# Kernel optimization log

Hardware: AMD Instinct MI355X
Metric: run time of the kernel (lower is better)

## Reference

```python
import jax, jax.numpy as jnp
import numpy as np

N_NODES = 100000
N_EDGES = 625000
D_FEAT = 128
OUT_DIM = 128


def setup_inputs() -> dict:
    key = jax.random.key(0)
    k1, k2, k3, k4 = jax.random.split(key, 4)
    feature = jax.random.normal(k1, (N_NODES, D_FEAT), dtype=jnp.float32)
    relation_weight = jax.random.uniform(k2, (N_EDGES, 1), dtype=jnp.float32)
    # row 0: destination (segment) ids, row 1: source (gather) ids
    relation_indices = jax.random.randint(k3, (2, N_EDGES), 0, N_NODES, dtype=jnp.int32)
    W = jax.random.normal(k4, (2 * D_FEAT, OUT_DIM), dtype=jnp.float32) * 0.05
    b = jnp.zeros((OUT_DIM,), dtype=jnp.float32)
    return {"feature": feature, "relation_weight": relation_weight, "W": W, "b": b,
            "relation_indices": relation_indices}


def reference(feature, relation_weight, W, b, relation_indices):
    dst = relation_indices[0]  # segment ids [E]
    src = relation_indices[1]  # gather ids  [E]
    n = feature.shape[0]
    # message: gather neighbor features and weight per edge  [E, D]
    feat_n = feature[src] * relation_weight
    # segment mean over destination nodes (dropout_rate=0.0 -> identity)
    seg_sum = jax.ops.segment_sum(feat_n, dst, num_segments=n)          # [N, D]
    seg_cnt = jax.ops.segment_sum(jnp.ones((src.shape[0], 1), feat_n.dtype), dst,
                                  num_segments=n)                        # [N, 1]
    neigh_mean = seg_sum / jnp.maximum(seg_cnt, 1.0)
    # concat self + aggregated, dense update (activation/normalization = None)
    h = jnp.concatenate([feature, neigh_mean], axis=-1)                  # [N, 2D]
    return h @ W + b
```

## Files before the change

### kernel.cpp

```cpp
#include <hip/hip_runtime.h>

constexpr int N   = 100000;
constexpr int E   = 625000;
constexpr int DF  = 128;
constexpr int CAP = 32;

typedef __attribute__((ext_vector_type(8))) _Float16 f16x8;
typedef __attribute__((ext_vector_type(2))) __fp16 fp16x2_raw;
typedef __attribute__((ext_vector_type(4))) float f32x4;

__device__ inline unsigned pkh(float lo, float hi) {
    union { fp16x2_raw h; unsigned u; } c;
    c.h = __builtin_amdgcn_cvt_pkrtz(lo, hi);
    return c.u;
}

__device__ inline int swz(int row, int byteInRow) {
    return row * 128 + (byteInRow ^ ((row & 7) << 4));
}

__global__ __launch_bounds__(256) void prep(
    const float* __restrict__ feature, const float* __restrict__ W,
    int* __restrict__ cnt, unsigned short* __restrict__ wtb,
    unsigned short* __restrict__ fh)
{
    int t = blockIdx.x * 256 + threadIdx.x;
    int stride = gridDim.x * 256;
    for (int i = t; i < N; i += stride) cnt[i] = 0;
    for (int i = t; i < 256 * 64; i += stride) {
        int k = (2 * i) >> 7, c = (2 * i) & 127;
        float a = W[2 * i], b = W[2 * i + 1];
        wtb[(c)     * 256 + k] = (unsigned short)(pkh(a, a) & 0xFFFF);
        wtb[(c + 1) * 256 + k] = (unsigned short)(pkh(b, b) & 0xFFFF);
    }
    int n8 = N * DF / 8;
    for (int i = t; i < n8; i += stride) {
        float4 a = reinterpret_cast<const float4*>(feature)[2 * i];
        float4 b = reinterpret_cast<const float4*>(feature)[2 * i + 1];
        uint4 o;
        o.x = pkh(a.x, a.y); o.y = pkh(a.z, a.w);
        o.z = pkh(b.x, b.y); o.w = pkh(b.z, b.w);
        reinterpret_cast<uint4*>(fh)[i] = o;
    }
}

__global__ __launch_bounds__(256) void direct_bucket(
    const int* __restrict__ dst, const int* __restrict__ src,
    const float* __restrict__ rw,
    int* __restrict__ cnt, int2* pad)
{
    int e = blockIdx.x * 256 + threadIdx.x;
    if (e < E) {
        int d = dst[e];
        int p = atomicAdd(&cnt[d], 1);
        if (p < CAP) pad[d * CAP + p] = make_int2(src[e], __float_as_int(rw[e]));
    }
}

__global__ __launch_bounds__(256) void aggregate(
    const unsigned short* __restrict__ fh,
    const int2* pad, const int* __restrict__ cnt,
    unsigned short* nbf)
{
    int node = blockIdx.x * 4 + (threadIdx.x >> 6);
    if (node >= N) return;
    int lane = threadIdx.x & 63;
    int eslot = lane >> 4;
    int chunk = lane & 15;
    int deg = cnt[node];
    int degc = min(deg, CAP);
    const int2* ep = pad + (size_t)node * CAP;
    const uint4* fh4 = reinterpret_cast<const uint4*>(fh);

    float acc[8];
    #pragma unroll
    for (int q = 0; q < 8; ++q) acc[q] = 0.f;

    int i = eslot;
    int2 sw0 = (i     < degc) ? ep[i]     : make_int2(0, 0);
    int2 sw1 = (i + 4 < degc) ? ep[i + 4] : make_int2(0, 0);
    while (i < degc) {
        union { uint4 u; _Float16 h[8]; } c0, c1;
        c0.u = fh4[(size_t)sw0.x * 16 + chunk];
        c1.u = fh4[(size_t)sw1.x * 16 + chunk];
        int2 sw0n = (i + 8  < degc) ? ep[i + 8]  : make_int2(0, 0);
        int2 sw1n = (i + 12 < degc) ? ep[i + 12] : make_int2(0, 0);
        float w0 = __int_as_float(sw0.y);
        float w1 = __int_as_float(sw1.y);
        #pragma unroll
        for (int q = 0; q < 8; ++q) acc[q] = fmaf((float)c0.h[q], w0, acc[q]);
        #pragma unroll
        for (int q = 0; q < 8; ++q) acc[q] = fmaf((float)c1.h[q], w1, acc[q]);
        i += 8; sw0 = sw0n; sw1 = sw1n;
    }
    #pragma unroll
    for (int q = 0; q < 8; ++q) {
        acc[q] += __shfl_xor(acc[q], 16, 64);
        acc[q] += __shfl_xor(acc[q], 32, 64);
    }
    if (lane < 16) {
        float inv = 1.0f / fmaxf((float)deg, 1.0f);
        uint4 o;
        o.x = pkh(acc[0] * inv, acc[1] * inv);
        o.y = pkh(acc[2] * inv, acc[3] * inv);
        o.z = pkh(acc[4] * inv, acc[5] * inv);
        o.w = pkh(acc[6] * inv, acc[7] * inv);
        reinterpret_cast<uint4*>(nbf)[(size_t)node * 16 + chunk] = o;
    }
}

__global__ __launch_bounds__(256) void sage_gemm(
    const unsigned short* __restrict__ fh, const unsigned short* __restrict__ nbf,
    const unsigned short* __restrict__ wtb,
    const float* __restrict__ bias, float* __restrict__ out)
{
    __shared__ short As[128 * 64];
    __shared__ short Bs[128 * 64];

    const int tid = threadIdx.x;
    const int lane = tid & 63;
    const int wv = tid >> 6;
    const int wr = (wv >> 1) * 64;
    const int wc = (wv & 1) * 64;
    const int l15 = lane & 15;
    const int lg  = lane >> 4;
    const int rowBase = blockIdx.x * 128;

    f32x4 acc[4][4];
    #pragma unroll
    for (int mi = 0; mi < 4; ++mi)
        #pragma unroll
        for (int ni = 0; ni < 4; ++ni)
            acc[mi][ni] = f32x4{0.f, 0.f, 0.f, 0.f};

    #pragma unroll
    for (int kc = 0; kc < 4; ++kc) {
        const int kglob = kc * 64;
        const unsigned short* Aap = (kc < 2) ? fh : nbf;
        const int kbase = (kc & 1) * 64;
        #pragma unroll
        for (int it = 0; it < 4; ++it) {
            int i = it * 256 + tid;
            int r  = i >> 3;
            int c8 = i & 7;
            int grow = rowBase + r;
            int4 v = {0, 0, 0, 0};
            if (grow < N)
                v = *reinterpret_cast<const int4*>(&Aap[(size_t)grow * DF + kbase + c8 * 8]);
            *reinterpret_cast<int4*>(reinterpret_cast<char*>(As) + swz(r, c8 * 16)) = v;
        }
        #pragma unroll
        for (int it = 0; it < 4; ++it) {
            int i = it * 256 + tid;
            int c  = i >> 3;
            int k8 = i & 7;
            int4 v = *reinterpret_cast<const int4*>(&wtb[(size_t)c * 256 + kglob + k8 * 8]);
            *reinterpret_cast<int4*>(reinterpret_cast<char*>(Bs) + swz(c, k8 * 16)) = v;
        }
        __syncthreads();

        #pragma unroll
        for (int kk = 0; kk < 2; ++kk) {
            const int kb = kk * 64;
            f16x8 af[4], bfr[4];
            #pragma unroll
            for (int mi = 0; mi < 4; ++mi) {
                int row = wr + mi * 16 + l15;
                af[mi] = *reinterpret_cast<const f16x8*>(
                    reinterpret_cast<const char*>(As) + swz(row, kb + lg * 16));
            }
            #pragma unroll
            for (int ni = 0; ni < 4; ++ni) {
                int col = wc + ni * 16 + l15;
                bfr[ni] = *reinterpret_cast<const f16x8*>(
                    reinterpret_cast<const char*>(Bs) + swz(col, kb + lg * 16));
            }
            #pragma unroll
            for (int mi = 0; mi < 4; ++mi)
                #pragma unroll
                for (int ni = 0; ni < 4; ++ni)
                    acc[mi][ni] = __builtin_amdgcn_mfma_f32_16x16x32_f16(
                        af[mi], bfr[ni], acc[mi][ni], 0, 0, 0);
        }
        __syncthreads();
    }

    #pragma unroll
    for (int ni = 0; ni < 4; ++ni) {
        int col = wc + ni * 16 + l15;
        float bc = bias[col];
        #pragma unroll
        for (int mi = 0; mi < 4; ++mi) {
            #pragma unroll
            for (int q = 0; q < 4; ++q) {
                int grow = rowBase + wr + mi * 16 + lg * 4 + q;
                if (grow < N) out[(size_t)grow * 128 + col] = acc[mi][ni][q] + bc;
            }
        }
    }
}

extern "C" void kernel_launch(void* const* d_in, const int* in_sizes, int n_in,
                              void* d_out, int out_size, void* d_ws, size_t ws_size,
                              hipStream_t stream) {
    const float* feature = (const float*)d_in[0];
    const float* rw      = (const float*)d_in[1];
    const float* W       = (const float*)d_in[2];
    const float* bias    = (const float*)d_in[3];
    const int*   ridx    = (const int*)d_in[4];
    const int*   dst     = ridx;
    const int*   src     = ridx + E;
    float* out = (float*)d_out;

    unsigned short* fh  = (unsigned short*)d_ws;
    int2*           pad = (int2*)(fh + (size_t)N * DF);
    unsigned short* nbf = (unsigned short*)pad;
    int*            cnt = (int*)((char*)pad + (size_t)N * CAP * 8);
    unsigned short* wtb = (unsigned short*)(cnt + N);

    prep<<<1280, 256, 0, stream>>>(feature, W, cnt, wtb, fh);
    direct_bucket<<<(E + 255) / 256, 256, 0, stream>>>(dst, src, rw, cnt, pad);
    aggregate<<<(N + 3) / 4, 256, 0, stream>>>(fh, pad, cnt, nbf);
    sage_gemm<<<(N + 127) / 128, 256, 0, stream>>>(fh, nbf, wtb, bias, out);
}
```

Baseline: 115.3 us.

## Stage full weight matrix in LDS once and stream A fragments from global

The GEMM now loads the whole 128x256 transposed weight into a 64KB LDS buffer once per block with a single barrier. A operands are read straight from global memory into registers instead of being staged through shared memory. Each wave now covers 32 rows by all 128 columns rather than 64x64. This removes the per-k-chunk barriers and A staging, at the cost of heavy LDS use that limits occupancy, and A loads that are strided per lane rather than coalesced.

```diff
diff --git a/kernel.cpp b/kernel.cpp
--- a/kernel.cpp
+++ b/kernel.cpp
@@ -114,83 +114,65 @@
     const unsigned short* __restrict__ wtb,
     const float* __restrict__ bias, float* __restrict__ out)
 {
-    __shared__ short As[128 * 64];
-    __shared__ short Bs[128 * 64];
+    __shared__ short Bs[128 * 256];
 
     const int tid = threadIdx.x;
     const int lane = tid & 63;
     const int wv = tid >> 6;
-    const int wr = (wv >> 1) * 64;
-    const int wc = (wv & 1) * 64;
     const int l15 = lane & 15;
     const int lg  = lane >> 4;
     const int rowBase = blockIdx.x * 128;
-
-    f32x4 acc[4][4];
-    #pragma unroll
-    for (int mi = 0; mi < 4; ++mi)
-        #pragma unroll
-        for (int ni = 0; ni < 4; ++ni)
+    const int wr = wv * 32;
+
+    #pragma unroll
+    for (int it = 0; it < 16; ++it) {
+        int i = it * 256 + tid;
+        int c  = i >> 5;
+        int k8 = i & 31;
+        int4 v = *reinterpret_cast<const int4*>(&wtb[(size_t)c * 256 + k8 * 8]);
+        *reinterpret_cast<int4*>(reinterpret_cast<char*>(Bs)
+            + c * 512 + ((k8 * 16) ^ ((c & 7) << 4))) = v;
+    }
+    __syncthreads();
+
+    const int row0 = rowBase + wr + l15;
+    const int row1 = row0 + 16;
+    const bool ok0 = row0 < N, ok1 = row1 < N;
+    const char* pf0 = (const char*)(fh  + (size_t)row0 * DF);
+    const char* pn0 = (const char*)(nbf + (size_t)row0 * DF);
+    const char* pf1 = (const char*)(fh  + (size_t)row1 * DF);
+    const char* pn1 = (const char*)(nbf + (size_t)row1 * DF);
+    const f16x8 zero = {};
+
+    f32x4 acc[2][8];
+    #pragma unroll
+    for (int mi = 0; mi < 2; ++mi)
+        #pragma unroll
+        for (int ni = 0; ni < 8; ++ni)
             acc[mi][ni] = f32x4{0.f, 0.f, 0.f, 0.f};
 
     #pragma unroll
-    for (int kc = 0; kc < 4; ++kc) {
-        const int kglob = kc * 64;
-        const unsigned short* Aap = (kc < 2) ? fh : nbf;
-        const int kbase = (kc & 1) * 64;
-        #pragma unroll
-        for (int it = 0; it < 4; ++it) {
-            int i = it * 256 + tid;
-            int r  = i >> 3;
-            int c8 = i & 7;
-            int grow = rowBase + r;
-            int4 v = {0, 0, 0, 0};
-            if (grow < N)
-                v = *reinterpret_cast<const int4*>(&Aap[(size_t)grow * DF + kbase + c8 * 8]);
-            *reinterpret_cast<int4*>(reinterpret_cast<char*>(As) + swz(r, c8 * 16)) = v;
+    for (int kk = 0; kk < 8; ++kk) {
+        const int kb = (kk & 3) * 64 + lg * 16;
+        f16x8 a0 = ok0 ? *reinterpret_cast<const f16x8*>((kk < 4 ? pf0 : pn0) + kb) : zero;
+        f16x8 a1 = ok1 ? *reinterpret_cast<const f16x8*>((kk < 4 ? pf1 : pn1) + kb) : zero;
+        const int kByte = kk * 64 + lg * 16;
+        #pragma unroll
+        for (int ni = 0; ni < 8; ++ni) {
+            int col = ni * 16 + l15;
+            f16x8 bf = *reinterpret_cast<const f16x8*>(
+                reinterpret_cast<const char*>(Bs) + col * 512 + (kByte ^ ((col & 7) << 4)));
+            acc[0][ni] = __builtin_amdgcn_mfma_f32_16x16x32_f16(a0, bf, acc[0][ni], 0, 0, 0);
+            acc[1][ni] = __builtin_amdgcn_mfma_f32_16x16x32_f16(a1, bf, acc[1][ni], 0, 0, 0);
         }
-        #pragma unroll
-        for (int it = 0; it < 4; ++it) {
-            int i = it * 256 + tid;
-            int c  = i >> 3;
-            int k8 = i & 7;
-            int4 v = *reinterpret_cast<const int4*>(&wtb[(size_t)c * 256 + kglob + k8 * 8]);
-            *reinterpret_cast<int4*>(reinterpret_cast<char*>(Bs) + swz(c, k8 * 16)) = v;
-        }
-        __syncthreads();
-
-        #pragma unroll
-        for (int kk = 0; kk < 2; ++kk) {
-            const int kb = kk * 64;
-            f16x8 af[4], bfr[4];
-            #pragma unroll
-            for (int mi = 0; mi < 4; ++mi) {
-                int row = wr + mi * 16 + l15;
-                af[mi] = *reinterpret_cast<const f16x8*>(
-                    reinterpret_cast<const char*>(As) + swz(row, kb + lg * 16));
-            }
-            #pragma unroll
-            for (int ni = 0; ni < 4; ++ni) {
-                int col = wc + ni * 16 + l15;
-                bfr[ni] = *reinterpret_cast<const f16x8*>(
-                    reinterpret_cast<const char*>(Bs) + swz(col, kb + lg * 16));
-            }
-            #pragma unroll
-            for (int mi = 0; mi < 4; ++mi)
-                #pragma unroll
-                for (int ni = 0; ni < 4; ++ni)
-                    acc[mi][ni] = __builtin_amdgcn_mfma_f32_16x16x32_f16(
-                        af[mi], bfr[ni], acc[mi][ni], 0, 0, 0);
-        }
-        __syncthreads();
-    }
-
-    #pragma unroll
-    for (int ni = 0; ni < 4; ++ni) {
-        int col = wc + ni * 16 + l15;
+    }
+
+    #pragma unroll
+    for (int ni = 0; ni < 8; ++ni) {
+        int col = ni * 16 + l15;
         float bc = bias[col];
         #pragma unroll
-        for (int mi = 0; mi < 4; ++mi) {
+        for (int mi = 0; mi < 2; ++mi) {
             #pragma unroll
             for (int q = 0; q < 4; ++q) {
                 int grow = rowBase + wr + mi * 16 + lg * 4 + q;
```

Result: faster. 112.5 us (-2.5%).
